# Kernel optimization log

Measured on AMD Instinct MI355X. Metric: run time of the kernel, lower is better.

Reference implementation:

```python
import jax, jax.numpy as jnp
import numpy as np

B, T, D, H = 2, 2048, 1024, 16
HD = D // H  # 64


def setup_inputs() -> dict:
    key = jax.random.key(0)
    ks = jax.random.split(key, 9)
    s = 1.0 / np.sqrt(D)
    return {
        "x": jax.random.normal(ks[0], (B, T, D), dtype=jnp.float32),
        "Wq": jax.random.uniform(ks[1], (D, D), minval=-s, maxval=s, dtype=jnp.float32),
        "bq": jax.random.uniform(ks[2], (D,), minval=-s, maxval=s, dtype=jnp.float32),
        "Wk": jax.random.uniform(ks[3], (D, D), minval=-s, maxval=s, dtype=jnp.float32),
        "bk": jax.random.uniform(ks[4], (D,), minval=-s, maxval=s, dtype=jnp.float32),
        "Wv": jax.random.uniform(ks[5], (D, D), minval=-s, maxval=s, dtype=jnp.float32),
        "bv": jax.random.uniform(ks[6], (D,), minval=-s, maxval=s, dtype=jnp.float32),
        "Wo": jax.random.uniform(ks[7], (D, D), minval=-s, maxval=s, dtype=jnp.float32),
        "bo": jax.random.uniform(ks[8], (D,), minval=-s, maxval=s, dtype=jnp.float32),
    }


def reference(x, Wq, bq, Wk, bk, Wv, bv, Wo, bo):
    b, t, d = x.shape
    # projections (nn.Linear: x @ W.T + b), split heads -> [B,H,T,hd]
    def split_heads(y):
        return y.reshape(b, t, H, HD).transpose(0, 2, 1, 3)
    Q = split_heads(x @ Wq.T + bq)
    K = split_heads(x @ Wk.T + bk)
    V = split_heads(x @ Wv.T + bv)
    # causal linear attention via cumulative outer-product state
    # Z[b,h,s,p,n] = V[b,h,s,p] * K[b,h,s,n]
    Z = jnp.einsum('bhsp,bhsn->bhspn', V, K)
    Z_cum = jnp.cumsum(Z, axis=2)  # prefix sum over time -> causal state
    Y = jnp.einsum('bhtn,bhtpn->bhtp', Q, Z_cum)  # [B,H,T,hd]
    Y = Y.transpose(0, 2, 1, 3).reshape(b, t, d)
    return Y @ Wo.T + bo
```

## Files before the change

### kernel.cpp

```cpp
#include <hip/hip_runtime.h>
#include <stdint.h>

#define B_  2
#define T_  2048
#define D_  1024
#define H_  16
#define HD_ 64
#define M_  (B_*T_)
#define CHK 128
#define NC  (T_/CHK)
#define BH  (B_*H_)

#define XN   4194304
#define WN   1048576

typedef unsigned short ushort_t;
typedef unsigned int   uint_t;

typedef __bf16 bf16x8 __attribute__((ext_vector_type(8)));
typedef float  f32x4  __attribute__((ext_vector_type(4)));

__device__ inline ushort_t f2bf(float f) {
    uint_t x = __float_as_uint(f);
    x += 0x7fffu + ((x >> 16) & 1u);
    return (ushort_t)(x >> 16);
}

__device__ inline uint4 pack8(const float4& lo, const float4& hi) {
    uint4 pk;
    pk.x = (uint_t)f2bf(lo.x) | ((uint_t)f2bf(lo.y) << 16);
    pk.y = (uint_t)f2bf(lo.z) | ((uint_t)f2bf(lo.w) << 16);
    pk.z = (uint_t)f2bf(hi.x) | ((uint_t)f2bf(hi.y) << 16);
    pk.w = (uint_t)f2bf(hi.z) | ((uint_t)f2bf(hi.w) << 16);
    return pk;
}

__global__ __launch_bounds__(256) void to_bf16_all(
    const float* __restrict__ x,  const float* __restrict__ Wq,
    const float* __restrict__ Wk, const float* __restrict__ Wv,
    const float* __restrict__ Wo, ushort_t* __restrict__ dst)
{
    const int idx = blockIdx.x * 256 + threadIdx.x;
    const int e   = idx * 8;
    const float* src;
    if      (e < XN)          src = x  + e;
    else if (e < XN + WN)     src = Wq + (e - XN);
    else if (e < XN + 2*WN)   src = Wk + (e - XN - WN);
    else if (e < XN + 3*WN)   src = Wv + (e - XN - 2*WN);
    else                      src = Wo + (e - XN - 3*WN);
    float4 lo = ((const float4*)src)[0];
    float4 hi = ((const float4*)src)[1];
    *(uint4*)(dst + e) = pack8(lo, hi);
}

__device__ inline void stage_rows(const ushort_t* __restrict__ g, ushort_t* ldsw,
                                  int lane, int issues) {
    const int rr  = lane >> 3;
    const int kg8 = ((lane & 7) ^ rr) << 3;
    const ushort_t* src = g + (size_t)rr * D_ + kg8;
    #pragma unroll
    for (int i = 0; i < issues; i++) {
        __builtin_amdgcn_global_load_lds(
            (const __attribute__((address_space(1))) void*)(src + (size_t)(i * 8) * D_),
            (__attribute__((address_space(3))) void*)(ldsw + i * 512),
            16, 0, 0);
    }
}

__global__ __launch_bounds__(256) void gemm_qkv(
    const ushort_t* __restrict__ xb, const ushort_t* __restrict__ Wqkvb,
    const float* __restrict__ bq, const float* __restrict__ bk,
    const float* __restrict__ bv, ushort_t* __restrict__ qkv_ws)
{
    const int flat = blockIdx.x;
    const int r    = flat & 7;
    const int j    = flat >> 3;
    const int mt   = ((r >> 1) << 4) | (j & 15);
    const int nt   = ((r & 1) << 2) | ((j >> 4) & 3);
    const int z    = j >> 6;

    const ushort_t* W  = Wqkvb + (size_t)z * WN;
    const float*    bi = (z == 0) ? bq : ((z == 1) ? bk : bv);
    ushort_t* out = qkv_ws + (size_t)z * (size_t)M_ * D_;

    __shared__ __align__(16) ushort_t As[64 * 64];
    __shared__ __align__(16) ushort_t Bs[128 * 64];

    const int tid  = threadIdx.x;
    const int m0   = mt * 64;
    const int n0   = nt * 128;
    const int wave = tid >> 6;
    const int lane = tid & 63;
    const int wm   = (wave >> 1) * 32;
    const int wn   = (wave & 1) * 64;
    const int fr   = lane & 15;
    const int quad = lane >> 4;

    const ushort_t* Ag = xb + (size_t)(m0 + wave * 16) * D_;
    const ushort_t* Bg = W  + (size_t)(n0 + wave * 32) * D_;
    ushort_t* Alds = &As[wave * 16 * 64];
    ushort_t* Blds = &Bs[wave * 32 * 64];

    f32x4 acc[2][4];
    #pragma unroll
    for (int i = 0; i < 2; i++)
        #pragma unroll
        for (int j2 = 0; j2 < 4; j2++)
            acc[i][j2] = (f32x4){0.f, 0.f, 0.f, 0.f};

    for (int k0 = 0; k0 < D_; k0 += 64) {
        __syncthreads();
        stage_rows(Ag + k0, Alds, lane, 2);
        stage_rows(Bg + k0, Blds, lane, 4);
        __syncthreads();

        #pragma unroll
        for (int ksg = 0; ksg <= 4; ksg += 4) {
            const int kgo = ((ksg + quad) ^ (fr & 7)) << 3;
            bf16x8 af[2], bf[4];
            #pragma unroll
            for (int i = 0; i < 2; i++) {
                uint4 u = *(const uint4*)&As[(wm + i * 16 + fr) * 64 + kgo];
                af[i] = __builtin_bit_cast(bf16x8, u);
            }
            #pragma unroll
            for (int j2 = 0; j2 < 4; j2++) {
                uint4 u = *(const uint4*)&Bs[(wn + j2 * 16 + fr) * 64 + kgo];
                bf[j2] = __builtin_bit_cast(bf16x8, u);
            }
            #pragma unroll
            for (int i = 0; i < 2; i++)
                #pragma unroll
                for (int j2 = 0; j2 < 4; j2++)
                    acc[i][j2] = __builtin_amdgcn_mfma_f32_16x16x32_bf16(
                        af[i], bf[j2], acc[i][j2], 0, 0, 0);
        }
    }

    const int rb = quad * 4;
    #pragma unroll
    for (int j2 = 0; j2 < 4; j2++) {
        const int n = n0 + wn + j2 * 16 + fr;
        const float bias = bi[n];
        const int h  = n >> 6;
        const int hd = n & 63;
        #pragma unroll
        for (int i = 0; i < 2; i++) {
            #pragma unroll
            for (int rr = 0; rr < 4; rr++) {
                const int m = m0 + wm + i * 16 + rb + rr;
                const int b = m >> 11, t = m & (T_ - 1);
                out[(((size_t)(b * H_ + h)) * T_ + t) * HD_ + hd] =
                    f2bf(acc[i][j2][rr] + bias);
            }
        }
    }
}

__global__ __launch_bounds__(256) void gemm_out(
    const ushort_t* __restrict__ Yw, const ushort_t* __restrict__ Wob,
    const float* __restrict__ bo, float* __restrict__ out)
{
    const int flat = blockIdx.x;
    const int r    = flat & 7;
    const int j    = flat >> 3;
    const int mt   = ((r >> 1) << 4) | (j & 15);
    const int nt   = ((r & 1) << 2) | (j >> 4);

    __shared__ __align__(16) ushort_t As[64 * 64];
    __shared__ __align__(16) ushort_t Bs[128 * 64];

    const int tid  = threadIdx.x;
    const int m0   = mt * 64;
    const int n0   = nt * 128;
    const int wave = tid >> 6;
    const int lane = tid & 63;
    const int wm   = (wave >> 1) * 32;
    const int wn   = (wave & 1) * 64;
    const int fr   = lane & 15;
    const int quad = lane >> 4;

    const ushort_t* Ag = Yw  + (size_t)(m0 + wave * 16) * D_;
    const ushort_t* Bg = Wob + (size_t)(n0 + wave * 32) * D_;
    ushort_t* Alds = &As[wave * 16 * 64];
    ushort_t* Blds = &Bs[wave * 32 * 64];

    f32x4 acc[2][4];
    #pragma unroll
    for (int i = 0; i < 2; i++)
        #pragma unroll
        for (int j2 = 0; j2 < 4; j2++)
            acc[i][j2] = (f32x4){0.f, 0.f, 0.f, 0.f};

    for (int k0 = 0; k0 < D_; k0 += 64) {
        __syncthreads();
        stage_rows(Ag + k0, Alds, lane, 2);
        stage_rows(Bg + k0, Blds, lane, 4);
        __syncthreads();

        #pragma unroll
        for (int ksg = 0; ksg <= 4; ksg += 4) {
            const int kgo = ((ksg + quad) ^ (fr & 7)) << 3;
            bf16x8 af[2], bf[4];
            #pragma unroll
            for (int i = 0; i < 2; i++) {
                uint4 u = *(const uint4*)&As[(wm + i * 16 + fr) * 64 + kgo];
                af[i] = __builtin_bit_cast(bf16x8, u);
            }
            #pragma unroll
            for (int j2 = 0; j2 < 4; j2++) {
                uint4 u = *(const uint4*)&Bs[(wn + j2 * 16 + fr) * 64 + kgo];
                bf[j2] = __builtin_bit_cast(bf16x8, u);
            }
            #pragma unroll
            for (int i = 0; i < 2; i++)
                #pragma unroll
                for (int j2 = 0; j2 < 4; j2++)
                    acc[i][j2] = __builtin_amdgcn_mfma_f32_16x16x32_bf16(
                        af[i], bf[j2], acc[i][j2], 0, 0, 0);
        }
    }

    const int rb = quad * 4;
    #pragma unroll
    for (int j2 = 0; j2 < 4; j2++) {
        const int n = n0 + wn + j2 * 16 + fr;
        const float bias = bo[n];
        #pragma unroll
        for (int i = 0; i < 2; i++) {
            #pragma unroll
            for (int rr = 0; rr < 4; rr++) {
                const int m = m0 + wm + i * 16 + rb + rr;
                out[(size_t)m * D_ + n] = acc[i][j2][rr] + bias;
            }
        }
    }
}

#define LDS_ 136

__device__ inline void scatter_T(const uint4* u, ushort_t* dst, int tid) {
    #pragma unroll
    for (int g = 0; g < 4; g++) {
        const int v  = tid + 256 * g;
        const int s  = v >> 3;
        const int p8 = (v & 7) * 8;
        ushort_t e[8];
        *(uint4*)e = u[g];
        const int sb = s >> 3, slo = s & 7;
        #pragma unroll
        for (int j = 0; j < 8; j++) {
            const int p   = p8 + j;
            const int blk = (sb & 8) | ((sb ^ (p >> 3)) & 7);
            dst[p * LDS_ + (blk << 3) + slo] = e[j];
        }
    }
}

__device__ inline void stage_T(const ushort_t* __restrict__ src, ushort_t* dst, int tid) {
    uint4 u[4];
    #pragma unroll
    for (int g = 0; g < 4; g++) u[g] = ((const uint4*)src)[tid + 256 * g];
    scatter_T(u, dst, tid);
}

__global__ __launch_bounds__(256) void chunk_states(
    const ushort_t* __restrict__ k_ws, const ushort_t* __restrict__ v_ws,
    ushort_t* __restrict__ states_bf)
{
    const int jn = blockIdx.x;
    const int bh = blockIdx.y;
    __shared__ __align__(16) ushort_t VtS[2][64 * LDS_];
    __shared__ __align__(16) ushort_t KtS[2][16 * LDS_];

    const int tid  = threadIdx.x;
    const int wave = tid >> 6, lane = tid & 63;
    const int fr = lane & 15, quad = lane >> 4, rb = quad * 4;
    const int p  = wave * 16 + fr;

    const ushort_t* kb = k_ws + (size_t)bh * T_ * HD_ + jn * 16;
    const uint4*    vp = (const uint4*)(v_ws + (size_t)bh * T_ * HD_);

    const int ks = tid >> 1;
    const int ng = (tid & 1) * 8;

    uint4 kv = *(const uint4*)(kb + ks * HD_ + ng);
    uint4 vv[4];
    #pragma unroll
    for (int g = 0; g < 4; g++) vv[g] = vp[tid + 256 * g];

    f32x4 accs = (f32x4){0.f, 0.f, 0.f, 0.f};

    for (int c = 0; c < NC; c++) {
        const int buf = c & 1;
        scatter_T(vv, VtS[buf], tid);
        {
            ushort_t e[8];
            *(uint4*)e = kv;
            const int sb = ks >> 3, slo = ks & 7;
            #pragma unroll
            for (int j = 0; j < 8; j++) {
                const int nl  = ng + j;
                const int blk = (sb & 8) | ((sb ^ (nl >> 3)) & 7);
                KtS[buf][nl * LDS_ + (blk << 3) + slo] = e[j];
            }
        }
        __syncthreads();

        if (c + 1 < NC) {
            kv = *(const uint4*)(kb + (size_t)(c + 1) * CHK * HD_ + ks * HD_ + ng);
            const int off = (c + 1) * 1024;
            #pragma unroll
            for (int g = 0; g < 4; g++) vv[g] = vp[off + tid + 256 * g];
        }

        ushort_t* sp = states_bf + ((size_t)bh * NC + c) * 4096;
        #pragma unroll
        for (int r = 0; r < 4; r++)
            sp[(wave * 16 + rb + r) * 64 + jn * 16 + fr] = f2bf(accs[r]);

        #pragma unroll
        for (int kt = 0; kt < 4; kt++) {
            const int sb   = kt * 4 + quad;
            const int blkA = (sb & 8) | ((sb ^ (p >> 3)) & 7);
            bf16x8 af = __builtin_bit_cast(bf16x8,
                *(const uint4*)&VtS[buf][p * LDS_ + (blkA << 3)]);
            const int blkB = (sb & 8) | ((sb ^ (fr >> 3)) & 7);
            uint4 ub = *(const uint4*)&KtS[buf][fr * LDS_ + (blkB << 3)];
            accs = __builtin_amdgcn_mfma_f32_16x16x32_bf16(
                af, __builtin_bit_cast(bf16x8, ub), accs, 0, 0, 0);
        }
    }
}

__global__ __launch_bounds__(256) void attn_chunk(
    const ushort_t* __restrict__ q_ws, const ushort_t* __restrict__ k_ws,
    const ushort_t* __restrict__ v_ws, const ushort_t* __restrict__ states_bf,
    ushort_t* __restrict__ y_ws)
{
    const int c = blockIdx.x, bh = blockIdx.y;
    __shared__ __align__(16) ushort_t VtS[64 * LDS_];
    __shared__ __align__(16) ushort_t Smat[128 * LDS_];

    const int tid  = threadIdx.x;
    const int wave = tid >> 6;
    const int lane = tid & 63;
    const int fr   = lane & 15;
    const int quad = lane >> 4;
    const int fk   = quad * 8;
    const int rb   = quad * 4;

    const size_t base = ((size_t)bh * T_ + (size_t)c * CHK) * HD_;
    const ushort_t* qg = q_ws + base;
    const ushort_t* kg = k_ws + base;
    const ushort_t* vg = v_ws + base;
    const ushort_t* st = states_bf + ((size_t)bh * NC + c) * 4096;

    stage_T(vg, VtS, tid);
    __syncthreads();

    const int mt[2] = { wave, 7 - wave };

    bf16x8 aq[2][2];
    #pragma unroll
    for (int i = 0; i < 2; i++)
        #pragma unroll
        for (int kk = 0; kk < 2; kk++) {
            uint4 u = *(const uint4*)(qg + (mt[i] * 16 + fr) * HD_ + kk * 32 + fk);
            aq[i][kk] = __builtin_bit_cast(bf16x8, u);
        }

    f32x4 acc[2][4];
    #pragma unroll
    for (int i = 0; i < 2; i++)
        #pragma unroll
        for (int jn = 0; jn < 4; jn++)
            acc[i][jn] = (f32x4){0.f, 0.f, 0.f, 0.f};

    #pragma unroll
    for (int jn = 0; jn < 4; jn++) {
        #pragma unroll
        for (int kk = 0; kk < 2; kk++) {
            uint4 u = *(const uint4*)(st + (jn * 16 + fr) * 64 + kk * 32 + fk);
            bf16x8 bsp = __builtin_bit_cast(bf16x8, u);
            #pragma unroll
            for (int i = 0; i < 2; i++)
                acc[i][jn] = __builtin_amdgcn_mfma_f32_16x16x32_bf16(
                    aq[i][kk], bsp, acc[i][jn], 0, 0, 0);
        }
    }

    #pragma unroll
    for (int i = 0; i < 2; i++) {
        const int m  = mt[i];
        const int nk = (m + 2) >> 1;
        const int jt = 2 * nk;

        f32x4 sc[8];
        #pragma unroll
        for (int j = 0; j < 8; j++) sc[j] = (f32x4){0.f, 0.f, 0.f, 0.f};

        #pragma unroll
        for (int j = 0; j < 8; j++) {
            if (j <= m) {
                #pragma unroll
                for (int kk = 0; kk < 2; kk++) {
                    uint4 u = *(const uint4*)(kg + (j * 16 + fr) * HD_ + kk * 32 + fk);
                    sc[j] = __builtin_amdgcn_mfma_f32_16x16x32_bf16(
                        aq[i][kk], __builtin_bit_cast(bf16x8, u), sc[j], 0, 0, 0);
                }
            }
        }

        #pragma unroll
        for (int j = 0; j < 8; j++) {
            if (j < jt) {
                f32x4 v = sc[j];
                if (j == m) {
                    #pragma unroll
                    for (int r = 0; r < 4; r++)
                        if (fr > rb + r) v[r] = 0.f;
                }
                #pragma unroll
                for (int r = 0; r < 4; r++)
                    Smat[(m * 16 + rb + r) * LDS_ + j * 16 + fr] = f2bf(v[r]);
            }
        }

        #pragma unroll
        for (int kt = 0; kt < 4; kt++) {
            if (kt < nk) {
                uint4 ua = *(const uint4*)&Smat[(m * 16 + fr) * LDS_ + kt * 32 + fk];
                bf16x8 as_ = __builtin_bit_cast(bf16x8, ua);
                #pragma unroll
                for (int jn = 0; jn < 4; jn++) {
                    const int p   = jn * 16 + fr;
                    const int sb  = kt * 4 + quad;
                    const int blk = (sb & 8) | ((sb ^ (p >> 3)) & 7);
                    uint4 ub = *(const uint4*)&VtS[p * LDS_ + (blk << 3)];
                    acc[i][jn] = __builtin_amdgcn_mfma_f32_16x16x32_bf16(
                        as_, __builtin_bit_cast(bf16x8, ub), acc[i][jn], 0, 0, 0);
                }
            }
        }
    }

    const int b = bh >> 4, h = bh & 15;
    ushort_t* yg = y_ws + ((size_t)(b * T_ + c * CHK)) * D_ + h * 64;
    #pragma unroll
    for (int i = 0; i < 2; i++) {
        #pragma unroll
        for (int jn = 0; jn < 4; jn++) {
            #pragma unroll
            for (int r = 0; r < 4; r++) {
                const int t = mt[i] * 16 + rb + r;
                const int p = jn * 16 + fr;
                yg[(size_t)t * D_ + p] = f2bf(acc[i][jn][r]);
            }
        }
    }
}

extern "C" void kernel_launch(void* const* d_in, const int* in_sizes, int n_in,
                              void* d_out, int out_size, void* d_ws, size_t ws_size,
                              hipStream_t stream)
{
    const float* x  = (const float*)d_in[0];
    const float* Wq = (const float*)d_in[1];
    const float* bq = (const float*)d_in[2];
    const float* Wk = (const float*)d_in[3];
    const float* bk = (const float*)d_in[4];
    const float* Wv = (const float*)d_in[5];
    const float* bv = (const float*)d_in[6];
    const float* Wo = (const float*)d_in[7];
    const float* bo = (const float*)d_in[8];
    float* out = (float*)d_out;

    ushort_t* cvt    = (ushort_t*)d_ws;
    ushort_t* xb     = cvt;
    ushort_t* Wqkvb  = cvt + (size_t)XN;
    ushort_t* Wob    = cvt + (size_t)XN + 3 * WN;
    ushort_t* q_ws   = cvt + (size_t)XN + 4 * WN;
    ushort_t* k_ws   = q_ws + (size_t)M_ * D_;
    ushort_t* v_ws   = k_ws + (size_t)M_ * D_;
    ushort_t* y_ws   = v_ws + (size_t)M_ * D_;
    ushort_t* states_bf = Wqkvb;

    to_bf16_all<<<dim3((XN + 4 * WN) / 8 / 256), 256, 0, stream>>>(
        x, Wq, Wk, Wv, Wo, cvt);
    gemm_qkv<<<dim3(1536), 256, 0, stream>>>(
        xb, Wqkvb, bq, bk, bv, q_ws);
    chunk_states<<<dim3(4, BH), 256, 0, stream>>>(k_ws, v_ws, states_bf);
    attn_chunk<<<dim3(NC, BH), 256, 0, stream>>>(q_ws, k_ws, v_ws, states_bf, y_ws);
    gemm_out<<<dim3(512), 256, 0, stream>>>(y_ws, Wob, bo, out);
}
```

Before: 176.6 us.

## Parallelize chunk state computation and use 512-thread attention blocks

```diff
diff --git a/kernel.cpp b/kernel.cpp
--- a/kernel.cpp
+++ b/kernel.cpp
@@ -264,76 +264,94 @@
     scatter_T(u, dst, tid);
 }
 
-__global__ __launch_bounds__(256) void chunk_states(
+__device__ inline void stage_T512(const ushort_t* __restrict__ src, ushort_t* dst, int tid) {
+    uint4 u[2];
+    #pragma unroll
+    for (int g = 0; g < 2; g++) u[g] = ((const uint4*)src)[tid + 512 * g];
+    #pragma unroll
+    for (int g = 0; g < 2; g++) {
+        const int v  = tid + 512 * g;
+        const int s  = v >> 3;
+        const int p8 = (v & 7) * 8;
+        ushort_t e[8];
+        *(uint4*)e = u[g];
+        const int sb = s >> 3, slo = s & 7;
+        #pragma unroll
+        for (int j = 0; j < 8; j++) {
+            const int p   = p8 + j;
+            const int blk = (sb & 8) | ((sb ^ (p >> 3)) & 7);
+            dst[p * LDS_ + (blk << 3) + slo] = e[j];
+        }
+    }
+}
+
+__global__ __launch_bounds__(256) void chunk_delta(
     const ushort_t* __restrict__ k_ws, const ushort_t* __restrict__ v_ws,
-    ushort_t* __restrict__ states_bf)
-{
-    const int jn = blockIdx.x;
+    float* __restrict__ delta)
+{
+    const int c  = blockIdx.x;
     const int bh = blockIdx.y;
-    __shared__ __align__(16) ushort_t VtS[2][64 * LDS_];
-    __shared__ __align__(16) ushort_t KtS[2][16 * LDS_];
+    __shared__ __align__(16) ushort_t VtS[64 * LDS_];
+    __shared__ __align__(16) ushort_t KtS[64 * LDS_];
 
     const int tid  = threadIdx.x;
     const int wave = tid >> 6, lane = tid & 63;
     const int fr = lane & 15, quad = lane >> 4, rb = quad * 4;
     const int p  = wave * 16 + fr;
 
-    const ushort_t* kb = k_ws + (size_t)bh * T_ * HD_ + jn * 16;
-    const uint4*    vp = (const uint4*)(v_ws + (size_t)bh * T_ * HD_);
-
-    const int ks = tid >> 1;
-    const int ng = (tid & 1) * 8;
-
-    uint4 kv = *(const uint4*)(kb + ks * HD_ + ng);
-    uint4 vv[4];
-    #pragma unroll
-    for (int g = 0; g < 4; g++) vv[g] = vp[tid + 256 * g];
-
-    f32x4 accs = (f32x4){0.f, 0.f, 0.f, 0.f};
-
+    const size_t base = ((size_t)bh * T_ + (size_t)c * CHK) * HD_;
+    stage_T(v_ws + base, VtS, tid);
+    stage_T(k_ws + base, KtS, tid);
+    __syncthreads();
+
+    f32x4 acc[4];
+    #pragma unroll
+    for (int jn = 0; jn < 4; jn++) acc[jn] = (f32x4){0.f, 0.f, 0.f, 0.f};
+
+    #pragma unroll
+    for (int kt = 0; kt < 4; kt++) {
+        const int sb   = kt * 4 + quad;
+        const int blkA = (sb & 8) | ((sb ^ (p >> 3)) & 7);
+        bf16x8 af = __builtin_bit_cast(bf16x8,
+            *(const uint4*)&VtS[p * LDS_ + (blkA << 3)]);
+        #pragma unroll
+        for (int jn = 0; jn < 4; jn++) {
+            const int nr   = jn * 16 + fr;
+            const int blkB = (sb & 8) | ((sb ^ (nr >> 3)) & 7);
+            uint4 ub = *(const uint4*)&KtS[nr * LDS_ + (blkB << 3)];
+            acc[jn] = __builtin_amdgcn_mfma_f32_16x16x32_bf16(
+                af, __builtin_bit_cast(bf16x8, ub), acc[jn], 0, 0, 0);
+        }
+    }
+
+    float* dp = delta + ((size_t)bh * NC + c) * 4096;
+    #pragma unroll
+    for (int jn = 0; jn < 4; jn++)
+        #pragma unroll
+        for (int r = 0; r < 4; r++)
+            dp[(wave * 16 + rb + r) * 64 + jn * 16 + fr] = acc[jn][r];
+}
+
+__global__ __launch_bounds__(256) void states_prefix(
+    const float* __restrict__ delta, ushort_t* __restrict__ states_bf)
+{
+    const int qd = blockIdx.x;
+    const int bh = blockIdx.y;
+    const size_t b0 = (size_t)bh * NC * 4096 + qd * 1024 + threadIdx.x;
+
+    float s[4] = {0.f, 0.f, 0.f, 0.f};
+    #pragma unroll
     for (int c = 0; c < NC; c++) {
-        const int buf = c & 1;
-        scatter_T(vv, VtS[buf], tid);
-        {
-            ushort_t e[8];
-            *(uint4*)e = kv;
-            const int sb = ks >> 3, slo = ks & 7;
-            #pragma unroll
-            for (int j = 0; j < 8; j++) {
-                const int nl  = ng + j;
-                const int blk = (sb & 8) | ((sb ^ (nl >> 3)) & 7);
-                KtS[buf][nl * LDS_ + (blk << 3) + slo] = e[j];
-            }
-        }
-        __syncthreads();
-
-        if (c + 1 < NC) {
-            kv = *(const uint4*)(kb + (size_t)(c + 1) * CHK * HD_ + ks * HD_ + ng);
-            const int off = (c + 1) * 1024;
-            #pragma unroll
-            for (int g = 0; g < 4; g++) vv[g] = vp[off + tid + 256 * g];
-        }
-
-        ushort_t* sp = states_bf + ((size_t)bh * NC + c) * 4096;
-        #pragma unroll
-        for (int r = 0; r < 4; r++)
-            sp[(wave * 16 + rb + r) * 64 + jn * 16 + fr] = f2bf(accs[r]);
-
-        #pragma unroll
-        for (int kt = 0; kt < 4; kt++) {
-            const int sb   = kt * 4 + quad;
-            const int blkA = (sb & 8) | ((sb ^ (p >> 3)) & 7);
-            bf16x8 af = __builtin_bit_cast(bf16x8,
-                *(const uint4*)&VtS[buf][p * LDS_ + (blkA << 3)]);
-            const int blkB = (sb & 8) | ((sb ^ (fr >> 3)) & 7);
-            uint4 ub = *(const uint4*)&KtS[buf][fr * LDS_ + (blkB << 3)];
-            accs = __builtin_amdgcn_mfma_f32_16x16x32_bf16(
-                af, __builtin_bit_cast(bf16x8, ub), accs, 0, 0, 0);
-        }
-    }
-}
-
-__global__ __launch_bounds__(256) void attn_chunk(
+        #pragma unroll
+        for (int u = 0; u < 4; u++) {
+            const size_t o = b0 + (size_t)c * 4096 + u * 256;
+            states_bf[o] = f2bf(s[u]);
+            s[u] += delta[o];
+        }
+    }
+}
+
+__global__ __launch_bounds__(512) void attn_chunk(
     const ushort_t* __restrict__ q_ws, const ushort_t* __restrict__ k_ws,
     const ushort_t* __restrict__ v_ws, const ushort_t* __restrict__ states_bf,
     ushort_t* __restrict__ y_ws)
@@ -356,26 +374,21 @@
     const ushort_t* vg = v_ws + base;
     const ushort_t* st = states_bf + ((size_t)bh * NC + c) * 4096;
 
-    stage_T(vg, VtS, tid);
+    stage_T512(vg, VtS, tid);
     __syncthreads();
 
-    const int mt[2] = { wave, 7 - wave };
-
-    bf16x8 aq[2][2];
-    #pragma unroll
-    for (int i = 0; i < 2; i++)
-        #pragma unroll
-        for (int kk = 0; kk < 2; kk++) {
-            uint4 u = *(const uint4*)(qg + (mt[i] * 16 + fr) * HD_ + kk * 32 + fk);
-            aq[i][kk] = __builtin_bit_cast(bf16x8, u);
-        }
-
-    f32x4 acc[2][4];
-    #pragma unroll
-    for (int i = 0; i < 2; i++)
-        #pragma unroll
-        for (int jn = 0; jn < 4; jn++)
-            acc[i][jn] = (f32x4){0.f, 0.f, 0.f, 0.f};
+    const int m = wave;
+
+    bf16x8 aq[2];
+    #pragma unroll
+    for (int kk = 0; kk < 2; kk++) {
+        uint4 u = *(const uint4*)(qg + (m * 16 + fr) * HD_ + kk * 32 + fk);
+        aq[kk] = __builtin_bit_cast(bf16x8, u);
+    }
+
+    f32x4 acc[4];
+    #pragma unroll
+    for (int jn = 0; jn < 4; jn++) acc[jn] = (f32x4){0.f, 0.f, 0.f, 0.f};
 
     #pragma unroll
     for (int jn = 0; jn < 4; jn++) {
@@ -383,64 +396,58 @@
         for (int kk = 0; kk < 2; kk++) {
             uint4 u = *(const uint4*)(st + (jn * 16 + fr) * 64 + kk * 32 + fk);
             bf16x8 bsp = __builtin_bit_cast(bf16x8, u);
-            #pragma unroll
-            for (int i = 0; i < 2; i++)
-                acc[i][jn] = __builtin_amdgcn_mfma_f32_16x16x32_bf16(
-                    aq[i][kk], bsp, acc[i][jn], 0, 0, 0);
-        }
-    }
-
-    #pragma unroll
-    for (int i = 0; i < 2; i++) {
-        const int m  = mt[i];
-        const int nk = (m + 2) >> 1;
-        const int jt = 2 * nk;
-
-        f32x4 sc[8];
-        #pragma unroll
-        for (int j = 0; j < 8; j++) sc[j] = (f32x4){0.f, 0.f, 0.f, 0.f};
-
-        #pragma unroll
-        for (int j = 0; j < 8; j++) {
-            if (j <= m) {
-                #pragma unroll
-                for (int kk = 0; kk < 2; kk++) {
-                    uint4 u = *(const uint4*)(kg + (j * 16 + fr) * HD_ + kk * 32 + fk);
-                    sc[j] = __builtin_amdgcn_mfma_f32_16x16x32_bf16(
-                        aq[i][kk], __builtin_bit_cast(bf16x8, u), sc[j], 0, 0, 0);
-                }
-            }
-        }
-
-        #pragma unroll
-        for (int j = 0; j < 8; j++) {
-            if (j < jt) {
-                f32x4 v = sc[j];
-                if (j == m) {
-                    #pragma unroll
-                    for (int r = 0; r < 4; r++)
-                        if (fr > rb + r) v[r] = 0.f;
-                }
+            acc[jn] = __builtin_amdgcn_mfma_f32_16x16x32_bf16(
+                aq[kk], bsp, acc[jn], 0, 0, 0);
+        }
+    }
+
+    const int nk = (m + 2) >> 1;
+    const int jt = 2 * nk;
+
+    f32x4 sc[8];
+    #pragma unroll
+    for (int j = 0; j < 8; j++) sc[j] = (f32x4){0.f, 0.f, 0.f, 0.f};
+
+    #pragma unroll
+    for (int j = 0; j < 8; j++) {
+        if (j <= m) {
+            #pragma unroll
+            for (int kk = 0; kk < 2; kk++) {
+                uint4 u = *(const uint4*)(kg + (j * 16 + fr) * HD_ + kk * 32 + fk);
+                sc[j] = __builtin_amdgcn_mfma_f32_16x16x32_bf16(
+                    aq[kk], __builtin_bit_cast(bf16x8, u), sc[j], 0, 0, 0);
+            }
+        }
+    }
+
+    #pragma unroll
+    for (int j = 0; j < 8; j++) {
+        if (j < jt) {
+            f32x4 v = sc[j];
+            if (j == m) {
                 #pragma unroll
                 for (int r = 0; r < 4; r++)
-                    Smat[(m * 16 + rb + r) * LDS_ + j * 16 + fr] = f2bf(v[r]);
-            }
-        }
-
-        #pragma unroll
-        for (int kt = 0; kt < 4; kt++) {
-            if (kt < nk) {
-                uint4 ua = *(const uint4*)&Smat[(m * 16 + fr) * LDS_ + kt * 32 + fk];
-                bf16x8 as_ = __builtin_bit_cast(bf16x8, ua);
-                #pragma unroll
-                for (int jn = 0; jn < 4; jn++) {
-                    const int p   = jn * 16 + fr;
-                    const int sb  = kt * 4 + quad;
-                    const int blk = (sb & 8) | ((sb ^ (p >> 3)) & 7);
-                    uint4 ub = *(const uint4*)&VtS[p * LDS_ + (blk << 3)];
-                    acc[i][jn] = __builtin_amdgcn_mfma_f32_16x16x32_bf16(
-                        as_, __builtin_bit_cast(bf16x8, ub), acc[i][jn], 0, 0, 0);
-                }
+                    if (fr > rb + r) v[r] = 0.f;
+            }
+            #pragma unroll
+            for (int r = 0; r < 4; r++)
+                Smat[(m * 16 + rb + r) * LDS_ + j * 16 + fr] = f2bf(v[r]);
+        }
+    }
+
+    #pragma unroll
+    for (int kt = 0; kt < 4; kt++) {
+        if (kt < nk) {
+            uint4 ua = *(const uint4*)&Smat[(m * 16 + fr) * LDS_ + kt * 32 + fk];
+            bf16x8 as_ = __builtin_bit_cast(bf16x8, ua);
+            #pragma unroll
+            for (int jn = 0; jn < 4; jn++) {
+                const int p   = jn * 16 + fr;
+                const int sb  = kt * 4 + quad;
+                const int blk = (sb & 8) | ((sb ^ (p >> 3)) & 7);
+                uint4 ub = *(const uint4*)&VtS[p * LDS_ + (blk << 3)];
+                acc[jn] = __builtin_amdgcn_mfma_f32_16x16x32_bf16(
+                    as_, __builtin_bit_cast(bf16x8, ub), acc[jn], 0, 0, 0);
             }
         }
     }
@@ -448,15 +455,12 @@
     const int b = bh >> 4, h = bh & 15;
     ushort_t* yg = y_ws + ((size_t)(b * T_ + c * CHK)) * D_ + h * 64;
     #pragma unroll
-    for (int i = 0; i < 2; i++) {
-        #pragma unroll
-        for (int jn = 0; jn < 4; jn++) {
-            #pragma unroll
-            for (int r = 0; r < 4; r++) {
-                const int t = mt[i] * 16 + rb + r;
-                const int p = jn * 16 + fr;
-                yg[(size_t)t * D_ + p] = f2bf(acc[i][jn][r]);
-            }
+    for (int jn = 0; jn < 4; jn++) {
+        #pragma unroll
+        for (int r = 0; r < 4; r++) {
+            const int t = m * 16 + rb + r;
+            const int p = jn * 16 + fr;
+            yg[(size_t)t * D_ + p] = f2bf(acc[jn][r]);
         }
     }
 }
@@ -485,12 +489,14 @@
     ushort_t* v_ws   = k_ws + (size_t)M_ * D_;
     ushort_t* y_ws   = v_ws + (size_t)M_ * D_;
     ushort_t* states_bf = Wqkvb;
+    float*    delta  = (float*)(y_ws + (size_t)M_ * D_);
 
     to_bf16_all<<<dim3((XN + 4 * WN) / 8 / 256), 256, 0, stream>>>(
         x, Wq, Wk, Wv, Wo, cvt);
     gemm_qkv<<<dim3(1536), 256, 0, stream>>>(
         xb, Wqkvb, bq, bk, bv, q_ws);
-    chunk_states<<<dim3(4, BH), 256, 0, stream>>>(k_ws, v_ws, states_bf);
-    attn_chunk<<<dim3(NC, BH), 256, 0, stream>>>(q_ws, k_ws, v_ws, states_bf, y_ws);
+    chunk_delta<<<dim3(NC, BH), 256, 0, stream>>>(k_ws, v_ws, delta);
+    states_prefix<<<dim3(4, BH), 256, 0, stream>>>(delta, states_bf);
+    attn_chunk<<<dim3(NC, BH), 512, 0, stream>>>(q_ws, k_ws, v_ws, states_bf, y_ws);
     gemm_out<<<dim3(512), 256, 0, stream>>>(y_ws, Wob, bo, out);
 }
```

New measurement: 162.4 us. -8.1%, faster.
